# Kernel optimization log

Measured on AMD Instinct MI355X. Metric: run time of the kernel, lower is better.

The kernel has to match this reference:

```python
import jax, jax.numpy as jnp
import numpy as np

B, T, D = 4, 2048, 1024
H = 16
HD = D // H
NORM = float(np.sqrt(D))  # module uses sqrt(out_features), not sqrt(head_dim)


def setup_inputs() -> dict:
    key = jax.random.key(0)
    k1, k2, k3 = jax.random.split(key, 3)
    x = jax.random.normal(k1, (B, T, D), dtype=jnp.float32)
    w_qkv = jax.random.normal(k2, (D, 3 * D), dtype=jnp.float32) * (1.0 / np.sqrt(D))
    w_proj = jax.random.normal(k3, (D, D), dtype=jnp.float32) * (1.0 / np.sqrt(D))
    return {"x": x, "w_qkv": w_qkv, "w_proj": w_proj}


def reference(x, w_qkv, w_proj):
    b, t, _ = x.shape
    qkv = jnp.einsum('btd,de->bte', x, w_qkv)  # [B,T,3D]
    q, k, v = jnp.split(qkv, 3, axis=-1)
    # [B,H,T,HD]
    q = q.reshape(b, t, H, HD).transpose(0, 2, 1, 3)
    k = k.reshape(b, t, H, HD).transpose(0, 2, 1, 3)
    v = v.reshape(b, t, H, HD).transpose(0, 2, 1, 3)
    attn = jnp.einsum('bhqd,bhkd->bhqk', q, k) / NORM
    causal = jnp.tril(jnp.ones((t, t), dtype=bool))
    attn = jnp.where(causal[None, None], attn, -jnp.inf)
    attn = jax.nn.softmax(attn, axis=-1)
    y = jnp.einsum('bhqk,bhkd->bhqd', attn, v)
    out = y.transpose(0, 2, 1, 3).reshape(b, t, D)
    return jnp.einsum('btd,de->bte', out, w_proj)
```

## Files before the change

kernel.cpp:

```cpp
#include <hip/hip_runtime.h>
#include <hip/hip_bf16.h>
#include <cstdint>
#include <cstddef>

typedef __bf16 bfx8 __attribute__((ext_vector_type(8)));
typedef float  fx4  __attribute__((ext_vector_type(4)));
typedef float  fx16 __attribute__((ext_vector_type(16)));

#define MFMA_B16(a, b, c)  __builtin_amdgcn_mfma_f32_16x16x32_bf16((a), (b), (c), 0, 0, 0)
#define MFMA32(a, b, c)    __builtin_amdgcn_mfma_f32_32x32x16_bf16((a), (b), (c), 0, 0, 0)

#define GLD_LDS16(gsrc, ldst)                                                  \
  __builtin_amdgcn_global_load_lds(                                            \
      (const __attribute__((address_space(1))) void*)(gsrc),                   \
      (__attribute__((address_space(3))) void*)(ldst), 16, 0, 0)

static __device__ __forceinline__ unsigned short f2bf(float f) {
  union { float f; unsigned u; } v; v.f = f;
  unsigned r = v.u + 0x7fffu + ((v.u >> 16) & 1u);
  return (unsigned short)(r >> 16);
}

static __device__ __forceinline__ bfx8 ldb8(const unsigned short* p) {
  return *(const bfx8*)(const void*)p;
}

static __device__ __forceinline__ unsigned pk2(float lo, float hi) {
  __hip_bfloat162 h2 = __float22bfloat162_rn(make_float2(lo, hi));
  union { __hip_bfloat162 h; unsigned u; } c; c.h = h2; return c.u;
}

static __device__ __forceinline__ bfx8 scale8(bfx8 x, float s) {
  union { bfx8 v; unsigned u[4]; } a; a.v = x;
  union { bfx8 v; unsigned u[4]; } r;
#pragma unroll
  for (int j = 0; j < 4; ++j) {
    union { unsigned u; float f; } lo, hi;
    lo.u = a.u[j] << 16;
    hi.u = a.u[j] & 0xffff0000u;
    r.u[j] = pk2(lo.f * s, hi.f * s);
  }
  return r.v;
}

#define BB 4
#define TT 2048
#define DD 1024
#define HH 16
#define HD 64

__global__ void k_cast(const float* __restrict__ in, unsigned short* __restrict__ out, int n) {
  int i = (blockIdx.x * blockDim.x + threadIdx.x) * 4;
  int stride = gridDim.x * blockDim.x * 4;
  for (; i < n; i += stride) {
    float4 v = *(const float4*)(in + i);
    ushort4 o;
    o.x = f2bf(v.x); o.y = f2bf(v.y); o.z = f2bf(v.z); o.w = f2bf(v.w);
    *(ushort4*)(out + i) = o;
  }
}

__global__ void k_transpose(const float* __restrict__ in, unsigned short* __restrict__ out,
                            int R, int C) {
  __shared__ float tile[32][33];
  int c0 = blockIdx.x * 32, r0 = blockIdx.y * 32;
  int tx = threadIdx.x, ty = threadIdx.y;
#pragma unroll
  for (int dy = 0; dy < 32; dy += 8)
    tile[ty + dy][tx] = in[(size_t)(r0 + ty + dy) * C + (c0 + tx)];
  __syncthreads();
#pragma unroll
  for (int dy = 0; dy < 32; dy += 8)
    out[(size_t)(c0 + ty + dy) * R + (r0 + tx)] = f2bf(tile[tx][ty + dy]);
}

template <int EPI>
__global__ __launch_bounds__(256) void k_gemm(
    const unsigned short* __restrict__ A,
    const unsigned short* __restrict__ Bt,
    float* __restrict__ outf,
    int M, int N, int K,
    unsigned short* __restrict__ qb, unsigned short* __restrict__ kb,
    unsigned short* __restrict__ vtb) {
  constexpr int BM = 128, BN = 128, BK = 32;
  __shared__ __align__(16) unsigned short As[BM * BK];
  __shared__ __align__(16) unsigned short Bs[BN * BK];

  const int tid  = threadIdx.x;
  const int lane = tid & 63;
  const int w    = tid >> 6;
  const int wr   = w >> 1, wc = w & 1;
  const int n16  = lane & 15, g = lane >> 4;
  const int m0 = blockIdx.y * BM, n0 = blockIdx.x * BN;

  fx4 acc[4][4] = {};

  for (int k0 = 0; k0 < K; k0 += BK) {
#pragma unroll
    for (int iss = 0; iss < 2; ++iss) {
      int bo   = iss * 4096 + w * 1024 + lane * 16;
      int row  = bo >> 6;
      int colb = bo & 63;
      const char* srcA = (const char*)A  + ((size_t)(m0 + row) * K + k0) * 2 + colb;
      const char* srcB = (const char*)Bt + ((size_t)(n0 + row) * K + k0) * 2 + colb;
      GLD_LDS16(srcA, (char*)As + iss * 4096 + w * 1024);
      GLD_LDS16(srcB, (char*)Bs + iss * 4096 + w * 1024);
    }
    __syncthreads();

    bfx8 af[4], bf[4];
#pragma unroll
    for (int mi = 0; mi < 4; ++mi)
      af[mi] = *(const bfx8*)(const void*)&As[(wr * 64 + mi * 16 + n16) * BK + g * 8];
#pragma unroll
    for (int ni = 0; ni < 4; ++ni)
      bf[ni] = *(const bfx8*)(const void*)&Bs[(wc * 64 + ni * 16 + n16) * BK + g * 8];
#pragma unroll
    for (int mi = 0; mi < 4; ++mi)
#pragma unroll
      for (int ni = 0; ni < 4; ++ni)
        acc[mi][ni] = MFMA_B16(af[mi], bf[ni], acc[mi][ni]);
    __syncthreads();
  }

#pragma unroll
  for (int mi = 0; mi < 4; ++mi) {
#pragma unroll
    for (int ni = 0; ni < 4; ++ni) {
      int mrow = m0 + wr * 64 + mi * 16 + g * 4;
      int ncol = n0 + wc * 64 + ni * 16 + n16;
      if (EPI == 0) {
#pragma unroll
        for (int i = 0; i < 4; ++i)
          outf[(size_t)(mrow + i) * N + ncol] = acc[mi][ni][i];
      } else {
        int sec = ncol >> 10;
        int h   = (ncol >> 6) & 15;
        int d   = ncol & 63;
#pragma unroll
        for (int i = 0; i < 4; ++i) {
          int mm = mrow + i;
          int b  = mm >> 11;
          int t  = mm & 2047;
          unsigned short val = f2bf(acc[mi][ni][i]);
          if (sec == 0)
            qb[(((size_t)(b * HH + h) * TT + t) << 6) + d] = val;
          else if (sec == 1)
            kb[(((size_t)(b * HH + h) * TT + t) << 6) + d] = val;
          else
            vtb[((size_t)(b * HH + h) * HD + d) * TT + t] = val;
        }
      }
    }
  }
}

struct KVfrag { bfx8 k0, k1, k2, k3, v0, v1, v2, v3; };

static __device__ __forceinline__ void load_kv(
    KVfrag& f, const unsigned short* __restrict__ kbase,
    const unsigned short* __restrict__ vbase, int kv0) {
  const unsigned short* kr = kbase + (size_t)kv0 * HD;
  f.k0 = ldb8(kr);       f.k1 = ldb8(kr + 16);
  f.k2 = ldb8(kr + 32);  f.k3 = ldb8(kr + 48);
  const unsigned short* vr = vbase + kv0;
  f.v0 = ldb8(vr);            f.v1 = ldb8(vr + 16);
  f.v2 = ldb8(vr + 32 * TT);  f.v3 = ldb8(vr + 32 * TT + 16);
}

template <bool MASK>
static __device__ __forceinline__ void attn_tile(
    const KVfrag& f, const bfx8* qf, int lim, int hi,
    float& m, float& l, fx16& o0, fx16& o1) {
  fx16 s = {};
  s = MFMA32(f.k0, qf[0], s);
  s = MFMA32(f.k1, qf[1], s);
  s = MFMA32(f.k2, qf[2], s);
  s = MFMA32(f.k3, qf[3], s);

  float t[16];
#pragma unroll
  for (int r = 0; r < 16; ++r) {
    int koff = (r & 3) + 8 * (r >> 2);
    t[r] = (!MASK || koff <= lim) ? s[r] : -__builtin_inff();
  }
  float x0 = fmaxf(t[0], t[1]),   x1 = fmaxf(t[2], t[3]);
  float x2 = fmaxf(t[4], t[5]),   x3 = fmaxf(t[6], t[7]);
  float x4 = fmaxf(t[8], t[9]),   x5 = fmaxf(t[10], t[11]);
  float x6 = fmaxf(t[12], t[13]), x7 = fmaxf(t[14], t[15]);
  float y0 = fmaxf(x0, x1), y1 = fmaxf(x2, x3), y2 = fmaxf(x4, x5), y3 = fmaxf(x6, x7);
  float mx = fmaxf(fmaxf(y0, y1), fmaxf(y2, y3));

  bool need = mx > m + 8.0f;
  if (__ballot(need) != 0ull) {
    float mo   = fmaxf(mx, __shfl_xor(mx, 32));
    float mnew = fmaxf(m, mo);
    float alpha = __builtin_amdgcn_exp2f(m - mnew);
    m = mnew;
    l *= alpha;
#pragma unroll
    for (int r = 0; r < 16; ++r) { o0[r] *= alpha; o1[r] *= alpha; }
  }

  float p[16];
#pragma unroll
  for (int r = 0; r < 16; ++r) p[r] = __builtin_amdgcn_exp2f(t[r] - m);
  float s0 = (p[0] + p[1]) + (p[2] + p[3]);
  float s1 = (p[4] + p[5]) + (p[6] + p[7]);
  float s2 = (p[8] + p[9]) + (p[10] + p[11]);
  float s3 = (p[12] + p[13]) + (p[14] + p[15]);
  l += (s0 + s1) + (s2 + s3);

  union { unsigned u[4]; bfx8 v; } P0, P1;
#pragma unroll
  for (int c = 0; c < 2; ++c) {
    unsigned a0 = pk2(p[8*c+0], p[8*c+1]);
    unsigned a1 = pk2(p[8*c+2], p[8*c+3]);
    unsigned b0 = pk2(p[8*c+4], p[8*c+5]);
    unsigned b1 = pk2(p[8*c+6], p[8*c+7]);
    unsigned xa0 = __shfl_xor(a0, 32), xa1 = __shfl_xor(a1, 32);
    unsigned xb0 = __shfl_xor(b0, 32), xb1 = __shfl_xor(b1, 32);
    unsigned* U = c ? P1.u : P0.u;
    U[0] = hi ? xb0 : a0;
    U[1] = hi ? xb1 : a1;
    U[2] = hi ? b0 : xa0;
    U[3] = hi ? b1 : xa1;
  }
  o0 = MFMA32(f.v0, P0.v, o0);
  o0 = MFMA32(f.v1, P1.v, o0);
  o1 = MFMA32(f.v2, P0.v, o1);
  o1 = MFMA32(f.v3, P1.v, o1);
}

static __device__ __forceinline__ void run_qtile(
    int i, const unsigned short* __restrict__ qbb,
    const unsigned short* __restrict__ kbase,
    const unsigned short* __restrict__ vbase,
    unsigned short* __restrict__ ybase0,
    int l31, int hi) {
  const int q0 = i * 32;
  const float CL = 0.0450842346f;
  const unsigned short* qp = qbb + (size_t)(q0 + l31) * HD + hi * 8;
  bfx8 qf[4];
#pragma unroll
  for (int dc = 0; dc < 4; ++dc) qf[dc] = scale8(ldb8(qp + dc * 16), CL);

  fx16 o0 = {}, o1 = {};
  float m = -__builtin_inff(), l = 0.f;
  const int nt = i + 1;
  const int lim = l31 - 4 * hi;

  KVfrag A, B;
  load_kv(A, kbase, vbase, 0);
  int t = 0;
  for (; t + 2 <= nt - 1; t += 2) {
    load_kv(B, kbase, vbase, (t + 1) * 32);
    attn_tile<false>(A, qf, 0, hi, m, l, o0, o1);
    load_kv(A, kbase, vbase, (t + 2) * 32);
    attn_tile<false>(B, qf, 0, hi, m, l, o0, o1);
  }
  if (t == nt - 2) {
    load_kv(B, kbase, vbase, (t + 1) * 32);
    attn_tile<false>(A, qf, 0, hi, m, l, o0, o1);
    attn_tile<true>(B, qf, lim, hi, m, l, o0, o1);
  } else {
    attn_tile<true>(A, qf, lim, hi, m, l, o0, o1);
  }

  l += __shfl_xor(l, 32);
  float inv = 1.0f / l;
  unsigned short* yp = ybase0 + (size_t)(q0 + l31) * DD + 4 * hi;
#pragma unroll
  for (int g = 0; g < 4; ++g) {
    ushort4 s4;
    s4.x = f2bf(o0[4*g+0] * inv); s4.y = f2bf(o0[4*g+1] * inv);
    s4.z = f2bf(o0[4*g+2] * inv); s4.w = f2bf(o0[4*g+3] * inv);
    *(ushort4*)(yp + 8 * g) = s4;
    s4.x = f2bf(o1[4*g+0] * inv); s4.y = f2bf(o1[4*g+1] * inv);
    s4.z = f2bf(o1[4*g+2] * inv); s4.w = f2bf(o1[4*g+3] * inv);
    *(ushort4*)(yp + 32 + 8 * g) = s4;
  }
}

__global__ __launch_bounds__(256) void k_attn(
    const unsigned short* __restrict__ qb,
    const unsigned short* __restrict__ kb,
    const unsigned short* __restrict__ vtb,
    unsigned short* __restrict__ yb) {
  const int tid  = threadIdx.x;
  const int lane = tid & 63;
  const int w    = tid >> 6;
  const int l31  = lane & 31;
  const int hi   = lane >> 5;

  int blk = blockIdx.x;
  int j  = blk & 7;
  int h  = (blk >> 3) & 15;
  int b  = blk >> 7;
  const int i = j * 4 + w;
  const size_t bh = (size_t)b * HH + h;

  const unsigned short* qbb   = qb  + bh * TT * HD;
  const unsigned short* kbase = kb  + bh * TT * HD + (size_t)l31 * HD + hi * 8;
  const unsigned short* vbase = vtb + (bh * HD + l31) * TT + hi * 8;
  unsigned short* ybase0      = yb  + (size_t)b * TT * DD + h * HD;

#pragma unroll 1
  for (int pass = 0; pass < 2; ++pass) {
    int ii = pass ? (63 - i) : i;
    run_qtile(ii, qbb, kbase, vbase, ybase0, l31, hi);
  }
}

extern "C" void kernel_launch(void* const* d_in, const int* in_sizes, int n_in,
                              void* d_out, int out_size, void* d_ws, size_t ws_size,
                              hipStream_t stream) {
  const float* x      = (const float*)d_in[0];
  const float* w_qkv  = (const float*)d_in[1];
  const float* w_proj = (const float*)d_in[2];
  float* out = (float*)d_out;

  char* ws = (char*)d_ws;
  unsigned short* xb     = (unsigned short*)(ws);
  unsigned short* wqkvT  = (unsigned short*)(ws + (size_t)(16u << 20));
  unsigned short* wprojT = (unsigned short*)(ws + (size_t)(22u << 20));
  unsigned short* qb     = (unsigned short*)(ws + (size_t)(24u << 20));
  unsigned short* kb     = (unsigned short*)(ws + (size_t)(40u << 20));
  unsigned short* vtb    = (unsigned short*)(ws + (size_t)(56u << 20));
  unsigned short* yb     = xb;

  k_cast<<<4096, 256, 0, stream>>>(x, xb, BB * TT * DD);

  dim3 tb(32, 8);
  k_transpose<<<dim3(3 * DD / 32, DD / 32), tb, 0, stream>>>(w_qkv, wqkvT, DD, 3 * DD);
  k_transpose<<<dim3(DD / 32, DD / 32), tb, 0, stream>>>(w_proj, wprojT, DD, DD);

  k_gemm<1><<<dim3(3 * DD / 128, BB * TT / 128), 256, 0, stream>>>(
      xb, wqkvT, nullptr, BB * TT, 3 * DD, DD, qb, kb, vtb);

  k_attn<<<BB * HH * 8, 256, 0, stream>>>(qb, kb, vtb, yb);

  k_gemm<0><<<dim3(DD / 128, BB * TT / 128), 256, 0, stream>>>(
      yb, wprojT, out, BB * TT, DD, DD, nullptr, nullptr, nullptr);
}
```

Measured before the change: 261.5 us.

## Split each causal query tile's KV range across four waves and merge via LDS

Each block now handles one head's query-tile pair (i, 63-i), with its four waves each processing a quarter of the KV range for both tiles. The partial softmax states (m, l, unnormalized O in bf16) go to shared memory and are combined with log-sum-exp rescaling after a barrier. Grid size grows fourfold, and per-wave causal work is balanced, to increase parallelism and reduce tail imbalance. The costs are redundant Q loads, an LDS merge with a block-wide sync, and bf16 rounding of the partial outputs.

```diff
diff --git a/kernel.cpp b/kernel.cpp
--- a/kernel.cpp
+++ b/kernel.cpp
@@ -19,6 +19,10 @@
   union { float f; unsigned u; } v; v.f = f;
   unsigned r = v.u + 0x7fffu + ((v.u >> 16) & 1u);
   return (unsigned short)(r >> 16);
+}
+
+static __device__ __forceinline__ float bf2f(unsigned short s) {
+  union { unsigned u; float f; } v; v.u = ((unsigned)s) << 16; return v.f;
 }
 
 static __device__ __forceinline__ bfx8 ldb8(const unsigned short* p) {
@@ -232,61 +236,46 @@
   o1 = MFMA32(f.v3, P1.v, o1);
 }
 
-static __device__ __forceinline__ void run_qtile(
-    int i, const unsigned short* __restrict__ qbb,
+static __device__ __forceinline__ void run_range(
+    int t0, int t1, bool masked,
     const unsigned short* __restrict__ kbase,
     const unsigned short* __restrict__ vbase,
-    unsigned short* __restrict__ ybase0,
-    int l31, int hi) {
-  const int q0 = i * 32;
-  const float CL = 0.0450842346f;
-  const unsigned short* qp = qbb + (size_t)(q0 + l31) * HD + hi * 8;
-  bfx8 qf[4];
-#pragma unroll
-  for (int dc = 0; dc < 4; ++dc) qf[dc] = scale8(ldb8(qp + dc * 16), CL);
-
-  fx16 o0 = {}, o1 = {};
-  float m = -__builtin_inff(), l = 0.f;
-  const int nt = i + 1;
-  const int lim = l31 - 4 * hi;
+    const bfx8* qf, int lim, int hi,
+    float& m, float& l, fx16& o0, fx16& o1) {
+  m = -__builtin_inff(); l = 0.f;
+  o0 = fx16{}; o1 = fx16{};
+  if (t1 <= t0) return;
 
   KVfrag A, B;
-  load_kv(A, kbase, vbase, 0);
-  int t = 0;
-  for (; t + 2 <= nt - 1; t += 2) {
+  load_kv(A, kbase, vbase, t0 * 32);
+  int t = t0;
+  for (; t + 2 <= t1 - 1; t += 2) {
     load_kv(B, kbase, vbase, (t + 1) * 32);
     attn_tile<false>(A, qf, 0, hi, m, l, o0, o1);
     load_kv(A, kbase, vbase, (t + 2) * 32);
     attn_tile<false>(B, qf, 0, hi, m, l, o0, o1);
   }
-  if (t == nt - 2) {
+  if (t == t1 - 2) {
     load_kv(B, kbase, vbase, (t + 1) * 32);
     attn_tile<false>(A, qf, 0, hi, m, l, o0, o1);
-    attn_tile<true>(B, qf, lim, hi, m, l, o0, o1);
+    if (masked) attn_tile<true>(B, qf, lim, hi, m, l, o0, o1);
+    else        attn_tile<false>(B, qf, 0, hi, m, l, o0, o1);
   } else {
-    attn_tile<true>(A, qf, lim, hi, m, l, o0, o1);
-  }
-
+    if (masked) attn_tile<true>(A, qf, lim, hi, m, l, o0, o1);
+    else        attn_tile<false>(A, qf, 0, hi, m, l, o0, o1);
+  }
   l += __shfl_xor(l, 32);
-  float inv = 1.0f / l;
-  unsigned short* yp = ybase0 + (size_t)(q0 + l31) * DD + 4 * hi;
-#pragma unroll
-  for (int g = 0; g < 4; ++g) {
-    ushort4 s4;
-    s4.x = f2bf(o0[4*g+0] * inv); s4.y = f2bf(o0[4*g+1] * inv);
-    s4.z = f2bf(o0[4*g+2] * inv); s4.w = f2bf(o0[4*g+3] * inv);
-    *(ushort4*)(yp + 8 * g) = s4;
-    s4.x = f2bf(o1[4*g+0] * inv); s4.y = f2bf(o1[4*g+1] * inv);
-    s4.z = f2bf(o1[4*g+2] * inv); s4.w = f2bf(o1[4*g+3] * inv);
-    *(ushort4*)(yp + 32 + 8 * g) = s4;
-  }
-}
-
-__global__ __launch_bounds__(256) void k_attn(
+}
+
+__global__ __launch_bounds__(256, 4) void k_attn(
     const unsigned short* __restrict__ qb,
     const unsigned short* __restrict__ kb,
     const unsigned short* __restrict__ vtb,
     unsigned short* __restrict__ yb) {
+  __shared__ float m_s[8][64];
+  __shared__ float l_s[8][64];
+  __shared__ __align__(16) unsigned short o_s[8][64][32];
+
   const int tid  = threadIdx.x;
   const int lane = tid & 63;
   const int w    = tid >> 6;
@@ -294,21 +283,90 @@
   const int hi   = lane >> 5;
 
   int blk = blockIdx.x;
-  int j  = blk & 7;
-  int h  = (blk >> 3) & 15;
-  int b  = blk >> 7;
-  const int i = j * 4 + w;
+  int i   = blk & 31;
+  int h   = (blk >> 5) & 15;
+  int b   = blk >> 9;
   const size_t bh = (size_t)b * HH + h;
+  const int tiles[2] = { i, 63 - i };
 
   const unsigned short* qbb   = qb  + bh * TT * HD;
   const unsigned short* kbase = kb  + bh * TT * HD + (size_t)l31 * HD + hi * 8;
   const unsigned short* vbase = vtb + (bh * HD + l31) * TT + hi * 8;
   unsigned short* ybase0      = yb  + (size_t)b * TT * DD + h * HD;
 
+  const float CL = 0.0450842346f;
+  const int lim  = l31 - 4 * hi;
+
 #pragma unroll 1
-  for (int pass = 0; pass < 2; ++pass) {
-    int ii = pass ? (63 - i) : i;
-    run_qtile(ii, qbb, kbase, vbase, ybase0, l31, hi);
+  for (int job = 0; job < 2; ++job) {
+    const int tile    = tiles[job];
+    const int quarter = job ? (3 - w) : w;
+    const int slot    = job * 4 + quarter;
+    const int nt      = tile + 1;
+    const int t0 = (quarter * nt) >> 2;
+    const int t1 = ((quarter + 1) * nt) >> 2;
+    const bool masked = (quarter == 3);
+
+    const unsigned short* qp = qbb + (size_t)(tile * 32 + l31) * HD + hi * 8;
+    bfx8 qf[4];
+#pragma unroll
+    for (int dc = 0; dc < 4; ++dc) qf[dc] = scale8(ldb8(qp + dc * 16), CL);
+
+    float m, l;
+    fx16 o0, o1;
+    run_range(t0, t1, masked, kbase, vbase, qf, lim, hi, m, l, o0, o1);
+
+    m_s[slot][lane] = m;
+    l_s[slot][lane] = l;
+    unsigned short* op = &o_s[slot][lane][0];
+#pragma unroll
+    for (int g = 0; g < 4; ++g) {
+      ushort4 s4;
+      s4.x = f2bf(o0[4*g+0]); s4.y = f2bf(o0[4*g+1]);
+      s4.z = f2bf(o0[4*g+2]); s4.w = f2bf(o0[4*g+3]);
+      *(ushort4*)(op + 4 * g) = s4;
+      s4.x = f2bf(o1[4*g+0]); s4.y = f2bf(o1[4*g+1]);
+      s4.z = f2bf(o1[4*g+2]); s4.w = f2bf(o1[4*g+3]);
+      *(ushort4*)(op + 16 + 4 * g) = s4;
+    }
+  }
+
+  __syncthreads();
+
+  {
+    const int tt = w >> 1, hh = w & 1;
+    const int base = tt * 4;
+    float m0 = m_s[base + 0][lane], m1 = m_s[base + 1][lane];
+    float m2 = m_s[base + 2][lane], m3 = m_s[base + 3][lane];
+    float mm = fmaxf(fmaxf(m0, m1), fmaxf(m2, m3));
+    float a0 = __builtin_amdgcn_exp2f(m0 - mm);
+    float a1 = __builtin_amdgcn_exp2f(m1 - mm);
+    float a2 = __builtin_amdgcn_exp2f(m2 - mm);
+    float a3 = __builtin_amdgcn_exp2f(m3 - mm);
+    float ll = a0 * l_s[base + 0][lane] + a1 * l_s[base + 1][lane] +
+               a2 * l_s[base + 2][lane] + a3 * l_s[base + 3][lane];
+    float inv = 1.0f / ll;
+
+    float O[16];
+#pragma unroll
+    for (int j = 0; j < 16; ++j) O[j] = 0.f;
+#pragma unroll
+    for (int q = 0; q < 4; ++q) {
+      float aq = (q == 0) ? a0 : (q == 1) ? a1 : (q == 2) ? a2 : a3;
+      const unsigned short* op = &o_s[base + q][lane][hh * 16];
+#pragma unroll
+      for (int j = 0; j < 16; ++j) O[j] += aq * bf2f(op[j]);
+    }
+
+    const int q0 = tiles[tt] * 32;
+    unsigned short* yp = ybase0 + (size_t)(q0 + l31) * DD + 32 * hh + 4 * hi;
+#pragma unroll
+    for (int g = 0; g < 4; ++g) {
+      ushort4 s4;
+      s4.x = f2bf(O[4*g+0] * inv); s4.y = f2bf(O[4*g+1] * inv);
+      s4.z = f2bf(O[4*g+2] * inv); s4.w = f2bf(O[4*g+3] * inv);
+      *(ushort4*)(yp + 8 * g) = s4;
+    }
   }
 }
 
@@ -338,7 +396,7 @@
   k_gemm<1><<<dim3(3 * DD / 128, BB * TT / 128), 256, 0, stream>>>(
       xb, wqkvT, nullptr, BB * TT, 3 * DD, DD, qb, kb, vtb);
 
-  k_attn<<<BB * HH * 8, 256, 0, stream>>>(qb, kb, vtb, yb);
+  k_attn<<<BB * HH * 32, 256, 0, stream>>>(qb, kb, vtb, yb);
 
   k_gemm<0><<<dim3(DD / 128, BB * TT / 128), 256, 0, stream>>>(
       yb, wprojT, out, BB * TT, DD, DD, nullptr, nullptr, nullptr);
```

Measured after the change: 612.8 us. 134% more time.

## Rewrite GEMMs as 256x128 double-buffered 8-wave kernels with swizzled LDS

Applied to the files above, without the earlier changes.

Replaces the 128x128, BK=32 single-buffered GEMM with a 512-thread kernel that computes 256x128 tiles at BK=64. Global-to-LDS loads are double buffered, with explicit vmcnt waits and raw s_barrier in place of __syncthreads. An XOR swizzle on the LDS column offset is meant to avoid bank conflicts, and s_setprio is raised around the MFMA bursts. The goal is to hide memory latency and cut the number of barriers, at the cost of more LDS per block (96KB) and delicate hand-written synchronisation. The attention pass loop is also manually unrolled into two calls.

```diff
diff --git a/kernel.cpp b/kernel.cpp
--- a/kernel.cpp
+++ b/kernel.cpp
@@ -21,8 +21,8 @@
   return (unsigned short)(r >> 16);
 }
 
-static __device__ __forceinline__ bfx8 ldb8(const unsigned short* p) {
-  return *(const bfx8*)(const void*)p;
+static __device__ __forceinline__ bfx8 ldb8(const void* p) {
+  return *(const bfx8*)p;
 }
 
 static __device__ __forceinline__ unsigned pk2(float lo, float hi) {
@@ -74,65 +74,108 @@
     out[(size_t)(c0 + ty + dy) * R + (r0 + tx)] = f2bf(tile[tx][ty + dy]);
 }
 
+
+static __device__ __forceinline__ void stage_kt(
+    const char* __restrict__ Ab, const char* __restrict__ Bb, int K, int kt,
+    char* ldsA, char* ldsB, int tid, int w) {
+  const int r8 = tid >> 3;
+  const int cb = (tid & 7) * 16;
+#pragma unroll
+  for (int u = 0; u < 4; ++u) {
+    int row = u * 64 + r8;
+    int scb = cb ^ ((row & 4) << 3);
+    GLD_LDS16(Ab + ((size_t)row * K + kt * 64) * 2 + scb, ldsA + u * 8192 + w * 1024);
+  }
+#pragma unroll
+  for (int u = 0; u < 2; ++u) {
+    int row = u * 64 + r8;
+    int scb = cb ^ ((row & 4) << 3);
+    GLD_LDS16(Bb + ((size_t)row * K + kt * 64) * 2 + scb, ldsB + u * 8192 + w * 1024);
+  }
+}
+
 template <int EPI>
-__global__ __launch_bounds__(256) void k_gemm(
+__global__ __launch_bounds__(512) void k_gemm8(
     const unsigned short* __restrict__ A,
     const unsigned short* __restrict__ Bt,
     float* __restrict__ outf,
     int M, int N, int K,
     unsigned short* __restrict__ qb, unsigned short* __restrict__ kb,
     unsigned short* __restrict__ vtb) {
-  constexpr int BM = 128, BN = 128, BK = 32;
-  __shared__ __align__(16) unsigned short As[BM * BK];
-  __shared__ __align__(16) unsigned short Bs[BN * BK];
+  __shared__ __align__(16) unsigned short Ls[2][24576];
 
   const int tid  = threadIdx.x;
   const int lane = tid & 63;
   const int w    = tid >> 6;
-  const int wr   = w >> 1, wc = w & 1;
+  const int wr   = w >> 1;
+  const int wc   = w & 1;
   const int n16  = lane & 15, g = lane >> 4;
-  const int m0 = blockIdx.y * BM, n0 = blockIdx.x * BN;
+  const int m0 = blockIdx.y * 256, n0 = blockIdx.x * 128;
+
+  const char* Ab = (const char*)(A  + (size_t)m0 * K);
+  const char* Bb = (const char*)(Bt + (size_t)n0 * K);
+  const int NKT = K >> 6;
 
   fx4 acc[4][4] = {};
 
-  for (int k0 = 0; k0 < K; k0 += BK) {
-#pragma unroll
-    for (int iss = 0; iss < 2; ++iss) {
-      int bo   = iss * 4096 + w * 1024 + lane * 16;
-      int row  = bo >> 6;
-      int colb = bo & 63;
-      const char* srcA = (const char*)A  + ((size_t)(m0 + row) * K + k0) * 2 + colb;
-      const char* srcB = (const char*)Bt + ((size_t)(n0 + row) * K + k0) * 2 + colb;
-      GLD_LDS16(srcA, (char*)As + iss * 4096 + w * 1024);
-      GLD_LDS16(srcB, (char*)Bs + iss * 4096 + w * 1024);
+  stage_kt(Ab, Bb, K, 0, (char*)Ls[0], (char*)Ls[0] + 32768, tid, w);
+
+#pragma unroll 1
+  for (int kt = 0; kt < NKT; ++kt) {
+    if (kt + 1 < NKT) {
+      const int d1 = (kt + 1) & 1;
+      stage_kt(Ab, Bb, K, kt + 1, (char*)Ls[d1], (char*)Ls[d1] + 32768, tid, w);
+      asm volatile("s_waitcnt vmcnt(6)" ::: "memory");
+    } else {
+      asm volatile("s_waitcnt vmcnt(0)" ::: "memory");
     }
-    __syncthreads();
-
-    bfx8 af[4], bf[4];
-#pragma unroll
-    for (int mi = 0; mi < 4; ++mi)
-      af[mi] = *(const bfx8*)(const void*)&As[(wr * 64 + mi * 16 + n16) * BK + g * 8];
-#pragma unroll
-    for (int ni = 0; ni < 4; ++ni)
-      bf[ni] = *(const bfx8*)(const void*)&Bs[(wc * 64 + ni * 16 + n16) * BK + g * 8];
-#pragma unroll
-    for (int mi = 0; mi < 4; ++mi)
-#pragma unroll
-      for (int ni = 0; ni < 4; ++ni)
-        acc[mi][ni] = MFMA_B16(af[mi], bf[ni], acc[mi][ni]);
-    __syncthreads();
-  }
-
-#pragma unroll
-  for (int mi = 0; mi < 4; ++mi) {
-#pragma unroll
-    for (int ni = 0; ni < 4; ++ni) {
-      int mrow = m0 + wr * 64 + mi * 16 + g * 4;
-      int ncol = n0 + wc * 64 + ni * 16 + n16;
+    asm volatile("s_barrier" ::: "memory");
+
+    const char* La = (const char*)Ls[kt & 1];
+    const char* Lb = La + 32768;
+
+#pragma unroll
+    for (int ph = 0; ph < 2; ++ph) {
+      bfx8 af[2][2], bf[4][2];
+#pragma unroll
+      for (int mf2 = 0; mf2 < 2; ++mf2)
+#pragma unroll
+        for (int kk = 0; kk < 2; ++kk) {
+          int row = wr * 64 + (ph * 2 + mf2) * 16 + n16;
+          int cb  = kk * 64 + g * 16;
+          af[mf2][kk] = ldb8(La + row * 128 + (cb ^ ((row & 4) << 3)));
+        }
+#pragma unroll
+      for (int nf = 0; nf < 4; ++nf)
+#pragma unroll
+        for (int kk = 0; kk < 2; ++kk) {
+          int row = wc * 64 + nf * 16 + n16;
+          int cb  = kk * 64 + g * 16;
+          bf[nf][kk] = ldb8(Lb + row * 128 + (cb ^ ((row & 4) << 3)));
+        }
+      __builtin_amdgcn_s_setprio(1);
+#pragma unroll
+      for (int kk = 0; kk < 2; ++kk)
+#pragma unroll
+        for (int mf2 = 0; mf2 < 2; ++mf2)
+#pragma unroll
+          for (int nf = 0; nf < 4; ++nf)
+            acc[ph * 2 + mf2][nf] = MFMA_B16(af[mf2][kk], bf[nf][kk], acc[ph * 2 + mf2][nf]);
+      __builtin_amdgcn_s_setprio(0);
+      asm volatile("s_barrier" ::: "memory");
+    }
+  }
+
+#pragma unroll
+  for (int mf = 0; mf < 4; ++mf) {
+#pragma unroll
+    for (int nf = 0; nf < 4; ++nf) {
+      int mrow = m0 + wr * 64 + mf * 16 + g * 4;
+      int ncol = n0 + wc * 64 + nf * 16 + n16;
       if (EPI == 0) {
 #pragma unroll
         for (int i = 0; i < 4; ++i)
-          outf[(size_t)(mrow + i) * N + ncol] = acc[mi][ni][i];
+          outf[(size_t)(mrow + i) * N + ncol] = acc[mf][nf][i];
       } else {
         int sec = ncol >> 10;
         int h   = (ncol >> 6) & 15;
@@ -142,7 +185,7 @@
           int mm = mrow + i;
           int b  = mm >> 11;
           int t  = mm & 2047;
-          unsigned short val = f2bf(acc[mi][ni][i]);
+          unsigned short val = f2bf(acc[mf][nf][i]);
           if (sec == 0)
             qb[(((size_t)(b * HH + h) * TT + t) << 6) + d] = val;
           else if (sec == 1)
@@ -305,11 +348,8 @@
   const unsigned short* vbase = vtb + (bh * HD + l31) * TT + hi * 8;
   unsigned short* ybase0      = yb  + (size_t)b * TT * DD + h * HD;
 
-#pragma unroll 1
-  for (int pass = 0; pass < 2; ++pass) {
-    int ii = pass ? (63 - i) : i;
-    run_qtile(ii, qbb, kbase, vbase, ybase0, l31, hi);
-  }
+  run_qtile(i,      qbb, kbase, vbase, ybase0, l31, hi);
+  run_qtile(63 - i, qbb, kbase, vbase, ybase0, l31, hi);
 }
 
 extern "C" void kernel_launch(void* const* d_in, const int* in_sizes, int n_in,
@@ -335,11 +375,11 @@
   k_transpose<<<dim3(3 * DD / 32, DD / 32), tb, 0, stream>>>(w_qkv, wqkvT, DD, 3 * DD);
   k_transpose<<<dim3(DD / 32, DD / 32), tb, 0, stream>>>(w_proj, wprojT, DD, DD);
 
-  k_gemm<1><<<dim3(3 * DD / 128, BB * TT / 128), 256, 0, stream>>>(
+  k_gemm8<1><<<dim3(3 * DD / 128, BB * TT / 256), 512, 0, stream>>>(
       xb, wqkvT, nullptr, BB * TT, 3 * DD, DD, qb, kb, vtb);
 
   k_attn<<<BB * HH * 8, 256, 0, stream>>>(qb, kb, vtb, yb);
 
-  k_gemm<0><<<dim3(DD / 128, BB * TT / 128), 256, 0, stream>>>(
+  k_gemm8<0><<<dim3(DD / 128, BB * TT / 256), 512, 0, stream>>>(
       yb, wprojT, out, BB * TT, DD, DD, nullptr, nullptr, nullptr);
 }
```

New measurement: 277.8 us. 6.2% more time.
